# Kernel tuning notes

Hardware: AMD Instinct MI355X
Metric: run time of the kernel (lower is better)

Reference implementation:

```python
import jax, jax.numpy as jnp
import numpy as np

CROP = 14          # initial_crop_size
POOL_K = 2         # maxpool_kernel_size == maxpool_stride


def setup_inputs() -> dict:
    key = jax.random.key(0)
    k1, k2 = jax.random.split(key)
    features = jax.random.normal(k1, (1, 50, 50, 1024), dtype=jnp.float32)
    raw = jax.random.uniform(k2, (1, 300, 4), dtype=jnp.float32)
    # well-formed normalized boxes: y1<=y2, x1<=x2
    ys = jnp.sort(raw[..., 0::2], axis=-1)
    xs = jnp.sort(raw[..., 1::2], axis=-1)
    boxes = jnp.stack([ys[..., 0], xs[..., 0], ys[..., 1], xs[..., 1]], axis=-1)
    return {"features": features, "boxes": boxes}


def _crop_and_resize(feat, boxes, crop_size):
    # feat: [H, W, C]; boxes: [N, 4] normalized (y1, x1, y2, x2)
    # Matches tf.image.crop_and_resize bilinear semantics for crop_size > 1.
    H, W, _ = feat.shape
    y1, x1, y2, x2 = boxes[:, 0], boxes[:, 1], boxes[:, 2], boxes[:, 3]
    grid = jnp.arange(crop_size, dtype=feat.dtype)  # [S]
    # sample coordinates in source pixel space: [N, S]
    ys = y1[:, None] * (H - 1) + grid[None, :] * ((y2 - y1) * (H - 1) / (crop_size - 1))[:, None]
    xs = x1[:, None] * (W - 1) + grid[None, :] * ((x2 - x1) * (W - 1) / (crop_size - 1))[:, None]
    y0f = jnp.floor(ys)
    x0f = jnp.floor(xs)
    wy = (ys - y0f)[:, :, None, None]  # [N, S, 1, 1]
    wx = (xs - x0f)[:, None, :, None]  # [N, 1, S, 1]
    y0 = jnp.clip(y0f.astype(jnp.int32), 0, H - 1)
    y1i = jnp.clip(y0 + 1, 0, H - 1)
    x0 = jnp.clip(x0f.astype(jnp.int32), 0, W - 1)
    x1i = jnp.clip(x0 + 1, 0, W - 1)
    # four corner gathers -> [N, S, S, C]
    tl = feat[y0[:, :, None], x0[:, None, :]]
    tr = feat[y0[:, :, None], x1i[:, None, :]]
    bl = feat[y1i[:, :, None], x0[:, None, :]]
    br = feat[y1i[:, :, None], x1i[:, None, :]]
    top = tl + (tr - tl) * wx
    bot = bl + (br - bl) * wx
    return top + (bot - top) * wy


def reference(features, boxes):
    # features: [1, H, W, C]; boxes: [1, N, 4]
    crops = _crop_and_resize(features[0], boxes[0], CROP)  # [N, 14, 14, C]
    N, S, _, C = crops.shape
    P = S // POOL_K
    # 2x2 stride-2 max pool (kernel == stride, S even)
    pooled = crops.reshape(N, P, POOL_K, P, POOL_K, C).max(axis=(2, 4))  # [N, 7, 7, C]
    return pooled[None]  # [1, N, 7, 7, C]
```

## Files before the change

kernel.cpp:

```cpp
#include <hip/hip_runtime.h>
#include <math.h>

#define FH 50
#define FW 50
#define FC 1024
#define FC4 256
#define NBOX 300
#define PO 7
#define CHQ 4
#define NPIX (FH * FW * FC)
#define BF16_BYTES (NPIX * 2)

typedef float nat4 __attribute__((ext_vector_type(4)));

__device__ __forceinline__ nat4 lerp4(nat4 a, nat4 b, float w) {
    return a + (b - a) * w;
}
__device__ __forceinline__ nat4 max4(nat4 a, nat4 b) {
    nat4 r;
    r.x = fmaxf(a.x, b.x);
    r.y = fmaxf(a.y, b.y);
    r.z = fmaxf(a.z, b.z);
    r.w = fmaxf(a.w, b.w);
    return r;
}
__device__ __forceinline__ nat4 bf2f(uint2 u) {
    nat4 r;
    r.x = __uint_as_float(u.x << 16);
    r.y = __uint_as_float(u.x & 0xffff0000u);
    r.z = __uint_as_float(u.y << 16);
    r.w = __uint_as_float(u.y & 0xffff0000u);
    return r;
}
__device__ __forceinline__ unsigned bfpack(float a, float b) {
    unsigned ua = __float_as_uint(a);
    unsigned ub = __float_as_uint(b);
    ua += 0x7fffu + ((ua >> 16) & 1u);
    ub += 0x7fffu + ((ub >> 16) & 1u);
    return (ua >> 16) | (ub & 0xffff0000u);
}

__global__ __launch_bounds__(256) void cvt_kernel(
    const float* __restrict__ feat, unsigned* __restrict__ ws)
{
    const int i = blockIdx.x * 256 + threadIdx.x;
    const float4 v = reinterpret_cast<const float4*>(feat)[i];
    uint2 w;
    w.x = bfpack(v.x, v.y);
    w.y = bfpack(v.z, v.w);
    reinterpret_cast<uint2*>(ws)[i] = w;
}

template<int NR>
__device__ __forceinline__ void pool_rows(
    const uint2* __restrict__ f2, const int (&rows)[NR], int c,
    float basex, float stepx, float wyA, float wyB,
    nat4* __restrict__ obase)
{
    uint2 cur[NR][2], nxt[NR][2];
    int cc;
    {
        const float xf = floorf(basex);
        cc = min(max((int)xf, 0), FW - 1);
        const int x1 = min(cc + 1, FW - 1);
#pragma unroll
        for (int q = 0; q < NR; ++q) {
            cur[q][0] = f2[(rows[q] + cc) * FC4 + c];
            cur[q][1] = f2[(rows[q] + x1) * FC4 + c];
        }
    }

    nat4 m = (nat4)(-INFINITY);
    for (int ix = 0; ix < 2 * PO; ++ix) {
        int d = 0;
        if (ix < 2 * PO - 1) {
            const float xsn = basex + (float)(ix + 1) * stepx;
            const int nx0 = min(max((int)floorf(xsn), 0), FW - 1);
            const int nx1 = min(nx0 + 1, FW - 1);
            d = nx0 - cc;
            if (d == 1) {
#pragma unroll
                for (int q = 0; q < NR; ++q)
                    nxt[q][1] = f2[(rows[q] + nx1) * FC4 + c];
            } else if (d >= 2) {
#pragma unroll
                for (int q = 0; q < NR; ++q) {
                    nxt[q][0] = f2[(rows[q] + nx0) * FC4 + c];
                    nxt[q][1] = f2[(rows[q] + nx1) * FC4 + c];
                }
            }
            cc = nx0;
        }

        {
            const float xs = basex + (float)ix * stepx;
            const float wx = xs - floorf(xs);
            const nat4 a0 = lerp4(bf2f(cur[0][0]), bf2f(cur[0][1]), wx);
            const nat4 a1 = lerp4(bf2f(cur[1][0]), bf2f(cur[1][1]), wx);
            const nat4 vA = lerp4(a0, a1, wyA);
            nat4 vB;
            if constexpr (NR == 2) {
                vB = lerp4(a0, a1, wyB);
            } else if constexpr (NR == 3) {
                const nat4 a2 = lerp4(bf2f(cur[2][0]), bf2f(cur[2][1]), wx);
                vB = lerp4(a1, a2, wyB);
            } else {
                const nat4 a2 = lerp4(bf2f(cur[2][0]), bf2f(cur[2][1]), wx);
                const nat4 a3 = lerp4(bf2f(cur[3][0]), bf2f(cur[3][1]), wx);
                vB = lerp4(a2, a3, wyB);
            }
            m = max4(m, max4(vA, vB));
        }

        if (ix & 1) {
            __builtin_nontemporal_store(m, obase + (ix >> 1) * FC4);
            m = (nat4)(-INFINITY);
        }

        if (ix < 2 * PO - 1) {
            if (d == 1) {
#pragma unroll
                for (int q = 0; q < NR; ++q) { cur[q][0] = cur[q][1]; cur[q][1] = nxt[q][1]; }
            } else if (d >= 2) {
#pragma unroll
                for (int q = 0; q < NR; ++q) { cur[q][0] = nxt[q][0]; cur[q][1] = nxt[q][1]; }
            }
        }
    }
}

__global__ __launch_bounds__(64) void roi_pool_bf16_kernel(
    const unsigned* __restrict__ ws,
    const float* __restrict__ boxes,
    float* __restrict__ out)
{
    const int j    = blockIdx.x & 7;
    const int cq   = j & 3;
    const int g    = blockIdx.x >> 3;
    const int unit = g * 2 + (j >> 2);
    const int n    = unit / 7;
    const int py   = unit - n * 7;
    const int c    = cq * 64 + threadIdx.x;

    const float by1 = boxes[n * 4 + 0];
    const float bx1 = boxes[n * 4 + 1];
    const float by2 = boxes[n * 4 + 2];
    const float bx2 = boxes[n * 4 + 3];

    const float stepy = (by2 - by1) * (49.0f / 13.0f);
    const float stepx = (bx2 - bx1) * (49.0f / 13.0f);
    const float basey = by1 * 49.0f;
    const float basex = bx1 * 49.0f;

    const float ysA = basey + (float)(2 * py) * stepy;
    const float ysB = ysA + stepy;
    const float fA = floorf(ysA); const float wyA = ysA - fA;
    const float fB = floorf(ysB); const float wyB = ysB - fB;
    const int y0A = min(max((int)fA, 0), FH - 1); const int y1A = min(y0A + 1, FH - 1);
    const int y0B = min(max((int)fB, 0), FH - 1); const int y1B = min(y0B + 1, FH - 1);

    const uint2* __restrict__ f2 = reinterpret_cast<const uint2*>(ws);
    nat4* __restrict__ obase =
        reinterpret_cast<nat4*>(out) + (size_t)(n * (PO * PO) + py * PO) * FC4 + c;

    if (y0B == y0A) {
        const int rows[2] = {y0A * FW, y1A * FW};
        pool_rows<2>(f2, rows, c, basex, stepx, wyA, wyB, obase);
    } else if (y0B == y1A) {
        const int rows[3] = {y0A * FW, y1A * FW, y1B * FW};
        pool_rows<3>(f2, rows, c, basex, stepx, wyA, wyB, obase);
    } else {
        const int rows[4] = {y0A * FW, y1A * FW, y0B * FW, y1B * FW};
        pool_rows<4>(f2, rows, c, basex, stepx, wyA, wyB, obase);
    }
}

__global__ __launch_bounds__(64) void roi_pool_f32_kernel(
    const float* __restrict__ feat,
    const float* __restrict__ boxes,
    float* __restrict__ out)
{
    const int j = blockIdx.x & 7;
    const int k = blockIdx.x >> 3;
    const int n = j + 8 * (k / (PO * CHQ));
    if (n >= NBOX) return;
    const int r  = k % (PO * CHQ);
    const int py = r >> 2;
    const int cq = r & 3;
    const int c4 = cq * 64 + threadIdx.x;

    const float by1 = boxes[n * 4 + 0];
    const float bx1 = boxes[n * 4 + 1];
    const float by2 = boxes[n * 4 + 2];
    const float bx2 = boxes[n * 4 + 3];
    const float stepy = (by2 - by1) * (49.0f / 13.0f);
    const float stepx = (bx2 - bx1) * (49.0f / 13.0f);
    const float basey = by1 * 49.0f;
    const float basex = bx1 * 49.0f;
    const float ysA = basey + (float)(2 * py) * stepy;
    const float ysB = ysA + stepy;
    const float fA = floorf(ysA); const float wyA = ysA - fA;
    const float fB = floorf(ysB); const float wyB = ysB - fB;
    const int y0A = min(max((int)fA, 0), FH - 1); const int y1A = min(y0A + 1, FH - 1);
    const int y0B = min(max((int)fB, 0), FH - 1); const int y1B = min(y0B + 1, FH - 1);

    const nat4* __restrict__ f4 = reinterpret_cast<const nat4*>(feat);
    const int rA0 = y0A * FW, rA1 = y1A * FW, rB0 = y0B * FW, rB1 = y1B * FW;

    int cc = -1000;
    nat4 A00, A01, A10, A11, B00, B01, B10, B11;
    A00 = A01 = A10 = A11 = B00 = B01 = B10 = B11 = (nat4)0.0f;
    nat4 m = (nat4)(-INFINITY);
    nat4* __restrict__ obase =
        reinterpret_cast<nat4*>(out) + (size_t)(n * (PO * PO) + py * PO) * FC4 + c4;

    for (int ix = 0; ix < 2 * PO; ++ix) {
        const float xs = basex + (float)ix * stepx;
        const float xf = floorf(xs);
        const float wx = xs - xf;
        int x0 = min(max((int)xf, 0), FW - 1);
        const int x1 = min(x0 + 1, FW - 1);
        if (x0 != cc) {
            if (x0 == cc + 1) {
                A00 = A01; A10 = A11; B00 = B01; B10 = B11;
                A01 = f4[(rA0 + x1) * FC4 + c4];
                A11 = f4[(rA1 + x1) * FC4 + c4];
                B01 = f4[(rB0 + x1) * FC4 + c4];
                B11 = f4[(rB1 + x1) * FC4 + c4];
            } else {
                A00 = f4[(rA0 + x0) * FC4 + c4];
                A01 = f4[(rA0 + x1) * FC4 + c4];
                A10 = f4[(rA1 + x0) * FC4 + c4];
                A11 = f4[(rA1 + x1) * FC4 + c4];
                B00 = f4[(rB0 + x0) * FC4 + c4];
                B01 = f4[(rB0 + x1) * FC4 + c4];
                B10 = f4[(rB1 + x0) * FC4 + c4];
                B11 = f4[(rB1 + x1) * FC4 + c4];
            }
            cc = x0;
        }
        const nat4 vA = lerp4(lerp4(A00, A01, wx), lerp4(A10, A11, wx), wyA);
        const nat4 vB = lerp4(lerp4(B00, B01, wx), lerp4(B10, B11, wx), wyB);
        m = max4(m, max4(vA, vB));
        if (ix & 1) {
            __builtin_nontemporal_store(m, obase + (ix >> 1) * FC4);
            m = (nat4)(-INFINITY);
        }
    }
}

extern "C" void kernel_launch(void* const* d_in, const int* in_sizes, int n_in,
                              void* d_out, int out_size, void* d_ws, size_t ws_size,
                              hipStream_t stream) {
    (void)in_sizes; (void)n_in; (void)out_size;
    const float* feat  = (const float*)d_in[0];
    const float* boxes = (const float*)d_in[1];
    float* out = (float*)d_out;

    if (ws_size >= (size_t)BF16_BYTES) {
        unsigned* wsb = (unsigned*)d_ws;
        cvt_kernel<<<dim3(NPIX / 4 / 256), dim3(256), 0, stream>>>(feat, wsb);
        roi_pool_bf16_kernel<<<dim3(8 * 1050), dim3(64), 0, stream>>>(wsb, boxes, out);
    } else {
        roi_pool_f32_kernel<<<dim3(8 * 38 * PO * CHQ), dim3(64), 0, stream>>>(feat, boxes, out);
    }
}
```

Measured before the change: 96.58 us.

## Double-buffer bilinear corner loads two samples ahead in ROI pool kernel

Replaces the column-reuse sliding window, which skipped reloading shared corners but serialized loads behind data-dependent branches, with a fully unrolled two-slot software pipeline. Each sample's corners are now loaded independently, two samples ahead of use. This removes branchy control flow and exposes more memory-level parallelism, at the cost of reloading corners that adjacent samples share and holding more registers. It also adds a min-waves launch bound of 6 and uses nontemporal loads in the fp32-to-bf16 conversion kernel.

```diff
diff --git a/kernel.cpp b/kernel.cpp
--- a/kernel.cpp
+++ b/kernel.cpp
@@ -44,7 +44,8 @@
     const float* __restrict__ feat, unsigned* __restrict__ ws)
 {
     const int i = blockIdx.x * 256 + threadIdx.x;
-    const float4 v = reinterpret_cast<const float4*>(feat)[i];
+    const nat4 v = __builtin_nontemporal_load(
+        reinterpret_cast<const nat4*>(feat) + i);
     uint2 w;
     w.x = bfpack(v.x, v.y);
     w.y = bfpack(v.z, v.w);
@@ -52,84 +53,64 @@
 }
 
 template<int NR>
-__device__ __forceinline__ void pool_rows(
+__device__ __forceinline__ void pool_samples(
     const uint2* __restrict__ f2, const int (&rows)[NR], int c,
     float basex, float stepx, float wyA, float wyB,
     nat4* __restrict__ obase)
 {
-    uint2 cur[NR][2], nxt[NR][2];
-    int cc;
-    {
-        const float xf = floorf(basex);
-        cc = min(max((int)xf, 0), FW - 1);
-        const int x1 = min(cc + 1, FW - 1);
+    uint2 buf[2][NR][2];
+
+#pragma unroll
+    for (int p = 0; p < 2; ++p) {
+        const float xs = basex + (float)p * stepx;
+        const int x0 = min(max((int)floorf(xs), 0), FW - 1);
+        const int x1 = min(x0 + 1, FW - 1);
 #pragma unroll
         for (int q = 0; q < NR; ++q) {
-            cur[q][0] = f2[(rows[q] + cc) * FC4 + c];
-            cur[q][1] = f2[(rows[q] + x1) * FC4 + c];
+            buf[p][q][0] = f2[(rows[q] + x0) * FC4 + c];
+            buf[p][q][1] = f2[(rows[q] + x1) * FC4 + c];
         }
     }
 
     nat4 m = (nat4)(-INFINITY);
-    for (int ix = 0; ix < 2 * PO; ++ix) {
-        int d = 0;
-        if (ix < 2 * PO - 1) {
-            const float xsn = basex + (float)(ix + 1) * stepx;
-            const int nx0 = min(max((int)floorf(xsn), 0), FW - 1);
-            const int nx1 = min(nx0 + 1, FW - 1);
-            d = nx0 - cc;
-            if (d == 1) {
-#pragma unroll
-                for (int q = 0; q < NR; ++q)
-                    nxt[q][1] = f2[(rows[q] + nx1) * FC4 + c];
-            } else if (d >= 2) {
-#pragma unroll
-                for (int q = 0; q < NR; ++q) {
-                    nxt[q][0] = f2[(rows[q] + nx0) * FC4 + c];
-                    nxt[q][1] = f2[(rows[q] + nx1) * FC4 + c];
-                }
+#pragma unroll
+    for (int i = 0; i < 2 * PO; ++i) {
+        const int sl = i & 1;
+
+        {
+            const float xs = basex + (float)i * stepx;
+            const float wx = xs - floorf(xs);
+            nat4 a[NR];
+#pragma unroll
+            for (int q = 0; q < NR; ++q)
+                a[q] = lerp4(bf2f(buf[sl][q][0]), bf2f(buf[sl][q][1]), wx);
+            const nat4 vA = lerp4(a[0], a[1], wyA);
+            nat4 vB;
+            if constexpr (NR == 2)      vB = lerp4(a[0], a[1], wyB);
+            else if constexpr (NR == 3) vB = lerp4(a[1], a[2], wyB);
+            else                        vB = lerp4(a[2], a[3], wyB);
+            m = max4(m, max4(vA, vB));
+        }
+
+        if (i < 2 * PO - 2) {
+            const float xs2 = basex + (float)(i + 2) * stepx;
+            const int x0 = min(max((int)floorf(xs2), 0), FW - 1);
+            const int x1 = min(x0 + 1, FW - 1);
+#pragma unroll
+            for (int q = 0; q < NR; ++q) {
+                buf[sl][q][0] = f2[(rows[q] + x0) * FC4 + c];
+                buf[sl][q][1] = f2[(rows[q] + x1) * FC4 + c];
             }
-            cc = nx0;
-        }
-
-        {
-            const float xs = basex + (float)ix * stepx;
-            const float wx = xs - floorf(xs);
-            const nat4 a0 = lerp4(bf2f(cur[0][0]), bf2f(cur[0][1]), wx);
-            const nat4 a1 = lerp4(bf2f(cur[1][0]), bf2f(cur[1][1]), wx);
-            const nat4 vA = lerp4(a0, a1, wyA);
-            nat4 vB;
-            if constexpr (NR == 2) {
-                vB = lerp4(a0, a1, wyB);
-            } else if constexpr (NR == 3) {
-                const nat4 a2 = lerp4(bf2f(cur[2][0]), bf2f(cur[2][1]), wx);
-                vB = lerp4(a1, a2, wyB);
-            } else {
-                const nat4 a2 = lerp4(bf2f(cur[2][0]), bf2f(cur[2][1]), wx);
-                const nat4 a3 = lerp4(bf2f(cur[3][0]), bf2f(cur[3][1]), wx);
-                vB = lerp4(a2, a3, wyB);
-            }
-            m = max4(m, max4(vA, vB));
-        }
-
-        if (ix & 1) {
-            __builtin_nontemporal_store(m, obase + (ix >> 1) * FC4);
+        }
+
+        if (i & 1) {
+            __builtin_nontemporal_store(m, obase + (i >> 1) * FC4);
             m = (nat4)(-INFINITY);
         }
-
-        if (ix < 2 * PO - 1) {
-            if (d == 1) {
-#pragma unroll
-                for (int q = 0; q < NR; ++q) { cur[q][0] = cur[q][1]; cur[q][1] = nxt[q][1]; }
-            } else if (d >= 2) {
-#pragma unroll
-                for (int q = 0; q < NR; ++q) { cur[q][0] = nxt[q][0]; cur[q][1] = nxt[q][1]; }
-            }
-        }
-    }
-}
-
-__global__ __launch_bounds__(64) void roi_pool_bf16_kernel(
+    }
+}
+
+__global__ __launch_bounds__(64, 6) void roi_pool_bf16_kernel(
     const unsigned* __restrict__ ws,
     const float* __restrict__ boxes,
     float* __restrict__ out)
@@ -165,13 +146,13 @@
 
     if (y0B == y0A) {
         const int rows[2] = {y0A * FW, y1A * FW};
-        pool_rows<2>(f2, rows, c, basex, stepx, wyA, wyB, obase);
+        pool_samples<2>(f2, rows, c, basex, stepx, wyA, wyB, obase);
     } else if (y0B == y1A) {
         const int rows[3] = {y0A * FW, y1A * FW, y1B * FW};
-        pool_rows<3>(f2, rows, c, basex, stepx, wyA, wyB, obase);
+        pool_samples<3>(f2, rows, c, basex, stepx, wyA, wyB, obase);
     } else {
         const int rows[4] = {y0A * FW, y1A * FW, y0B * FW, y1B * FW};
-        pool_rows<4>(f2, rows, c, basex, stepx, wyA, wyB, obase);
+        pool_samples<4>(f2, rows, c, basex, stepx, wyA, wyB, obase);
     }
 }
 
```

Measured after the change: 100.6 us. 1.04x slower.
